# Performance work log

Hardware: AMD Instinct MI355X
Metric: run time of the kernel (lower is better)

The kernel has to match this reference:

```python
import jax, jax.numpy as jnp
import numpy as np

NIN = 4096
NOUT = 4096
LN_EPS = 1e-5  # torch.nn.LayerNorm default


def setup_inputs() -> dict:
    key = jax.random.key(0)
    ks = jax.random.split(key, 8)
    x = jax.random.normal(ks[0], (1, NIN), dtype=jnp.float32)
    hid = jax.random.normal(ks[1], (1, NOUT), dtype=jnp.float32)
    hebb = jnp.zeros((NOUT, NOUT), dtype=jnp.float32) + 1e-6  # initialZeroHebb
    # parameters
    w_in = 0.01 * jax.random.normal(ks[2], (NOUT, NIN), dtype=jnp.float32)  # inp_lin weight (no bias)
    w = 0.01 * jnp.eye(NOUT, NOUT, dtype=jnp.float32)                        # Plastic.w
    alpha = 0.01 * jax.random.normal(ks[3], (NOUT, NOUT), dtype=jnp.float32)
    b = 0.01 * jax.random.normal(ks[4], (NOUT,), dtype=jnp.float32)
    lamda = 0.01 * jnp.ones((1,), dtype=jnp.float32)
    pred_eta = 0.01 * jax.random.normal(ks[5], (NOUT, NOUT), dtype=jnp.float32)
    pred_eta_b = 0.01 * jax.random.normal(ks[6], (NOUT,), dtype=jnp.float32)
    ln_gamma = jnp.ones((NOUT,), dtype=jnp.float32)
    ln_beta = jnp.zeros((NOUT,), dtype=jnp.float32)
    return {"x": x, "hid": hid, "hebb": hebb, "w_in": w_in, "w": w,
            "alpha": alpha, "b": b, "lamda": lamda, "pred_eta": pred_eta,
            "pred_eta_b": pred_eta_b, "ln_gamma": ln_gamma, "ln_beta": ln_beta}


def reference(x, hid, hebb, w_in, w, alpha, b, lamda, pred_eta, pred_eta_b, ln_gamma, ln_beta):
    # Cell.forward (nonlin = ReLU for both wx and the post-LN output)
    wx = jax.nn.relu(x @ w_in.T)                       # [1, nout]
    wh = hid @ (w + alpha * hebb) + b                  # Plastic.forward, [1, nout]
    s = wx + wh
    mu = jnp.mean(s, axis=-1, keepdims=True)
    var = jnp.mean((s - mu) ** 2, axis=-1, keepdims=True)
    ln = ln_gamma * (s - mu) * jax.lax.rsqrt(var + LN_EPS) + ln_beta
    wy = jax.nn.relu(ln)                               # new hidden state, [1, nout]
    # Plastic.update_hebb(x=hid, y=wh, hebb)
    eta_hat = jax.nn.sigmoid(wh @ pred_eta + pred_eta_b)           # [1, nout]
    outer = hid[0, :, None] * wh[0, None, :]                        # [nout, nout]
    hebb_new = (1.0 - lamda) * hebb + eta_hat.T * outer             # row i scaled by eta_hat[0, i]
    return wy, hebb_new
```

## Files before the change

### kernel.cpp

```cpp
#include <hip/hip_runtime.h>
#include <hip/hip_bf16.h>
#include <math.h>

#define N 4096

__inline__ __device__ float waveReduceSum(float v) {
    #pragma unroll
    for (int o = 32; o > 0; o >>= 1) v += __shfl_down(v, o);
    return v;
}

__global__ __launch_bounds__(256) void k_wx(const float* __restrict__ x,
                                            const float* __restrict__ w_in,
                                            float* __restrict__ wx_out) {
    int j = blockIdx.x;
    const float4* row = reinterpret_cast<const float4*>(w_in + (size_t)j * N);
    const float4* xv  = reinterpret_cast<const float4*>(x);
    float sum = 0.f;
    #pragma unroll 4
    for (int k = threadIdx.x; k < N / 4; k += 256) {
        float4 a = row[k], c = xv[k];
        sum += a.x * c.x + a.y * c.y + a.z * c.z + a.w * c.w;
    }
    sum = waveReduceSum(sum);
    __shared__ float wsum[4];
    int wid = threadIdx.x >> 6, lane = threadIdx.x & 63;
    if (lane == 0) wsum[wid] = sum;
    __syncthreads();
    if (threadIdx.x == 0) {
        float t = wsum[0] + wsum[1] + wsum[2] + wsum[3];
        wx_out[j] = fmaxf(t, 0.f);
    }
}

__global__ __launch_bounds__(256) void k_wh_part(const float* __restrict__ hid,
                                                 const float* __restrict__ w,
                                                 const float* __restrict__ alpha,
                                                 const float* __restrict__ hebb,
                                                 float* __restrict__ part) {
    int j  = blockIdx.x * 256 + threadIdx.x;
    int i0 = blockIdx.y * 64;
    float sum = 0.f;
    #pragma unroll 4
    for (int i = i0; i < i0 + 64; ++i) {
        size_t off = (size_t)i * N + j;
        sum = fmaf(hid[i], fmaf(alpha[off], hebb[off], w[off]), sum);
    }
    part[(size_t)blockIdx.y * N + j] = sum;
}

__global__ __launch_bounds__(1024) void k_ln(const float* __restrict__ part,
                                             const float* __restrict__ b,
                                             const float* __restrict__ wx,
                                             const float* __restrict__ gamma,
                                             const float* __restrict__ beta,
                                             float* __restrict__ wh_out,
                                             float* __restrict__ wy_out) {
    __shared__ float red[16];
    __shared__ float bc[2];
    int tid = threadIdx.x;
    int wid = tid >> 6, lane = tid & 63;
    float sv[4];
    float lsum = 0.f;
    #pragma unroll
    for (int q = 0; q < 4; ++q) {
        int j = q * 1024 + tid;
        float acc = b[j];
        for (int c = 0; c < 64; ++c) acc += part[(size_t)c * N + j];
        wh_out[j] = acc;
        float s = acc + wx[j];
        sv[q] = s;
        lsum += s;
    }
    float wv = waveReduceSum(lsum);
    if (lane == 0) red[wid] = wv;
    __syncthreads();
    if (tid < 64) {
        float t = (tid < 16) ? red[tid] : 0.f;
        t = waveReduceSum(t);
        if (tid == 0) bc[0] = t * (1.f / N);
    }
    __syncthreads();
    float mean = bc[0];
    __syncthreads();
    float lsq = 0.f;
    #pragma unroll
    for (int q = 0; q < 4; ++q) { float d = sv[q] - mean; lsq += d * d; }
    wv = waveReduceSum(lsq);
    if (lane == 0) red[wid] = wv;
    __syncthreads();
    if (tid < 64) {
        float t = (tid < 16) ? red[tid] : 0.f;
        t = waveReduceSum(t);
        if (tid == 0) bc[1] = t * (1.f / N);
    }
    __syncthreads();
    float rstd = rsqrtf(bc[1] + 1e-5f);
    #pragma unroll
    for (int q = 0; q < 4; ++q) {
        int j = q * 1024 + tid;
        float ln = fmaf(gamma[j] * (sv[q] - mean), rstd, beta[j]);
        wy_out[j] = fmaxf(ln, 0.f);
    }
}

__global__ __launch_bounds__(256) void k_eta_part(const float* __restrict__ wh,
                                                  const float* __restrict__ pe,
                                                  float* __restrict__ part) {
    int j  = blockIdx.x * 256 + threadIdx.x;
    int i0 = blockIdx.y * 64;
    float sum = 0.f;
    #pragma unroll 4
    for (int i = i0; i < i0 + 64; ++i) {
        sum = fmaf(wh[i], pe[(size_t)i * N + j], sum);
    }
    part[(size_t)blockIdx.y * N + j] = sum;
}

__global__ __launch_bounds__(256) void k_eta_fin(const float* __restrict__ part,
                                                 const float* __restrict__ pb,
                                                 float* __restrict__ eta) {
    int j = blockIdx.x * 256 + threadIdx.x;
    float s = pb[j];
    for (int c = 0; c < 64; ++c) s += part[(size_t)c * N + j];
    eta[j] = 1.f / (1.f + expf(-s));
}

__global__ __launch_bounds__(256) void k_hebb(const float* __restrict__ hebb,
                                              const float* __restrict__ eta,
                                              const float* __restrict__ hid,
                                              const float* __restrict__ wh,
                                              const float* __restrict__ lamda,
                                              float* __restrict__ out) {
    int i  = blockIdx.y;
    int j0 = blockIdx.x * 1024 + threadIdx.x * 4;
    float decay = 1.f - lamda[0];
    float coef  = eta[i] * hid[i];
    const float4 h  = *reinterpret_cast<const float4*>(hebb + (size_t)i * N + j0);
    const float4 w4 = *reinterpret_cast<const float4*>(wh + j0);
    float4 r;
    r.x = fmaf(decay, h.x, coef * w4.x);
    r.y = fmaf(decay, h.y, coef * w4.y);
    r.z = fmaf(decay, h.z, coef * w4.z);
    r.w = fmaf(decay, h.w, coef * w4.w);
    *reinterpret_cast<float4*>(out + (size_t)i * N + j0) = r;
}

extern "C" void kernel_launch(void* const* d_in, const int* in_sizes, int n_in,
                              void* d_out, int out_size, void* d_ws, size_t ws_size,
                              hipStream_t stream) {
    const float* x         = (const float*)d_in[0];
    const float* hid       = (const float*)d_in[1];
    const float* hebb      = (const float*)d_in[2];
    const float* w_in      = (const float*)d_in[3];
    const float* w         = (const float*)d_in[4];
    const float* alpha     = (const float*)d_in[5];
    const float* b         = (const float*)d_in[6];
    const float* lamda     = (const float*)d_in[7];
    const float* pred_eta  = (const float*)d_in[8];
    const float* pred_eta_b= (const float*)d_in[9];
    const float* ln_gamma  = (const float*)d_in[10];
    const float* ln_beta   = (const float*)d_in[11];

    float* wy       = (float*)d_out;
    float* hebb_out = (float*)d_out + N;

    float* ws   = (float*)d_ws;
    float* part = ws;
    float* wx   = ws + 64 * N;
    float* wh   = ws + 64 * N + N;
    float* eta  = ws + 64 * N + 2 * N;

    k_wx      <<<N, 256, 0, stream>>>(x, w_in, wx);
    k_wh_part <<<dim3(16, 64), 256, 0, stream>>>(hid, w, alpha, hebb, part);
    k_ln      <<<1, 1024, 0, stream>>>(part, b, wx, ln_gamma, ln_beta, wh, wy);
    k_eta_part<<<dim3(16, 64), 256, 0, stream>>>(wh, pred_eta, part);
    k_eta_fin <<<16, 256, 0, stream>>>(part, pred_eta_b, eta);
    k_hebb    <<<dim3(4, N), 256, 0, stream>>>(hebb, eta, hid, wh, lamda, hebb_out);
}
```

Baseline: 106.6 us.

## Vectorize split-K matvecs with float4, double chunk count, parallelize wh reduction

The column-wise split-K matvec kernels for wh and eta now load float4 per thread with 4 columns each and use 128 row chunks of 32 instead of 64 chunks of 64. The partial-sum reduction for wh moves out of the single-block layernorm kernel into its own 16-block kernel, so the serial 64-deep reduction in one block no longer sits on the critical path. The aim is wider memory transactions and more parallelism in the reductions, at the cost of one extra launch and twice the partial-buffer traffic.

```diff
diff --git a/kernel.cpp b/kernel.cpp
--- a/kernel.cpp
+++ b/kernel.cpp
@@ -3,6 +3,8 @@
 #include <math.h>
 
 #define N 4096
+#define CHUNK 32
+#define NCHUNK (N / CHUNK)
 
 __inline__ __device__ float waveReduceSum(float v) {
     #pragma unroll
@@ -17,7 +19,7 @@
     const float4* row = reinterpret_cast<const float4*>(w_in + (size_t)j * N);
     const float4* xv  = reinterpret_cast<const float4*>(x);
     float sum = 0.f;
-    #pragma unroll 4
+    #pragma unroll
     for (int k = threadIdx.x; k < N / 4; k += 256) {
         float4 a = row[k], c = xv[k];
         sum += a.x * c.x + a.y * c.y + a.z * c.z + a.w * c.w;
@@ -38,23 +40,41 @@
                                                  const float* __restrict__ alpha,
                                                  const float* __restrict__ hebb,
                                                  float* __restrict__ part) {
-    int j  = blockIdx.x * 256 + threadIdx.x;
-    int i0 = blockIdx.y * 64;
-    float sum = 0.f;
+    int j0 = blockIdx.x * 1024 + threadIdx.x * 4;
+    int i0 = blockIdx.y * CHUNK;
+    const float4* w4 = reinterpret_cast<const float4*>(w);
+    const float4* a4 = reinterpret_cast<const float4*>(alpha);
+    const float4* h4 = reinterpret_cast<const float4*>(hebb);
+    float4 acc = make_float4(0.f, 0.f, 0.f, 0.f);
     #pragma unroll 4
-    for (int i = i0; i < i0 + 64; ++i) {
-        size_t off = (size_t)i * N + j;
-        sum = fmaf(hid[i], fmaf(alpha[off], hebb[off], w[off]), sum);
-    }
-    part[(size_t)blockIdx.y * N + j] = sum;
-}
-
-__global__ __launch_bounds__(1024) void k_ln(const float* __restrict__ part,
-                                             const float* __restrict__ b,
+    for (int i = i0; i < i0 + CHUNK; ++i) {
+        size_t idx = ((size_t)i * N + j0) >> 2;
+        float4 wv = w4[idx];
+        float4 av = a4[idx];
+        float4 hv = h4[idx];
+        float  h  = hid[i];
+        acc.x = fmaf(h, fmaf(av.x, hv.x, wv.x), acc.x);
+        acc.y = fmaf(h, fmaf(av.y, hv.y, wv.y), acc.y);
+        acc.z = fmaf(h, fmaf(av.z, hv.z, wv.z), acc.z);
+        acc.w = fmaf(h, fmaf(av.w, hv.w, wv.w), acc.w);
+    }
+    *reinterpret_cast<float4*>(part + (size_t)blockIdx.y * N + j0) = acc;
+}
+
+__global__ __launch_bounds__(256) void k_wh_fin(const float* __restrict__ part,
+                                                const float* __restrict__ b,
+                                                float* __restrict__ wh) {
+    int j = blockIdx.x * 256 + threadIdx.x;
+    float s = b[j];
+    #pragma unroll 8
+    for (int c = 0; c < NCHUNK; ++c) s += part[(size_t)c * N + j];
+    wh[j] = s;
+}
+
+__global__ __launch_bounds__(1024) void k_ln(const float* __restrict__ wh,
                                              const float* __restrict__ wx,
                                              const float* __restrict__ gamma,
                                              const float* __restrict__ beta,
-                                             float* __restrict__ wh_out,
                                              float* __restrict__ wy_out) {
     __shared__ float red[16];
     __shared__ float bc[2];
@@ -65,10 +85,7 @@
     #pragma unroll
     for (int q = 0; q < 4; ++q) {
         int j = q * 1024 + tid;
-        float acc = b[j];
-        for (int c = 0; c < 64; ++c) acc += part[(size_t)c * N + j];
-        wh_out[j] = acc;
-        float s = acc + wx[j];
+        float s = wh[j] + wx[j];
         sv[q] = s;
         lsum += s;
     }
@@ -107,14 +124,21 @@
 __global__ __launch_bounds__(256) void k_eta_part(const float* __restrict__ wh,
                                                   const float* __restrict__ pe,
                                                   float* __restrict__ part) {
-    int j  = blockIdx.x * 256 + threadIdx.x;
-    int i0 = blockIdx.y * 64;
-    float sum = 0.f;
+    int j0 = blockIdx.x * 1024 + threadIdx.x * 4;
+    int i0 = blockIdx.y * CHUNK;
+    const float4* p4 = reinterpret_cast<const float4*>(pe);
+    float4 acc = make_float4(0.f, 0.f, 0.f, 0.f);
     #pragma unroll 4
-    for (int i = i0; i < i0 + 64; ++i) {
-        sum = fmaf(wh[i], pe[(size_t)i * N + j], sum);
-    }
-    part[(size_t)blockIdx.y * N + j] = sum;
+    for (int i = i0; i < i0 + CHUNK; ++i) {
+        size_t idx = ((size_t)i * N + j0) >> 2;
+        float4 pv = p4[idx];
+        float  h  = wh[i];
+        acc.x = fmaf(h, pv.x, acc.x);
+        acc.y = fmaf(h, pv.y, acc.y);
+        acc.z = fmaf(h, pv.z, acc.z);
+        acc.w = fmaf(h, pv.w, acc.w);
+    }
+    *reinterpret_cast<float4*>(part + (size_t)blockIdx.y * N + j0) = acc;
 }
 
 __global__ __launch_bounds__(256) void k_eta_fin(const float* __restrict__ part,
@@ -122,7 +146,8 @@
                                                  float* __restrict__ eta) {
     int j = blockIdx.x * 256 + threadIdx.x;
     float s = pb[j];
-    for (int c = 0; c < 64; ++c) s += part[(size_t)c * N + j];
+    #pragma unroll 8
+    for (int c = 0; c < NCHUNK; ++c) s += part[(size_t)c * N + j];
     eta[j] = 1.f / (1.f + expf(-s));
 }
 
@@ -167,14 +192,15 @@
 
     float* ws   = (float*)d_ws;
     float* part = ws;
-    float* wx   = ws + 64 * N;
-    float* wh   = ws + 64 * N + N;
-    float* eta  = ws + 64 * N + 2 * N;
+    float* wx   = ws + NCHUNK * N;
+    float* wh   = ws + NCHUNK * N + N;
+    float* eta  = ws + NCHUNK * N + 2 * N;
 
     k_wx      <<<N, 256, 0, stream>>>(x, w_in, wx);
-    k_wh_part <<<dim3(16, 64), 256, 0, stream>>>(hid, w, alpha, hebb, part);
-    k_ln      <<<1, 1024, 0, stream>>>(part, b, wx, ln_gamma, ln_beta, wh, wy);
-    k_eta_part<<<dim3(16, 64), 256, 0, stream>>>(wh, pred_eta, part);
+    k_wh_part <<<dim3(4, NCHUNK), 256, 0, stream>>>(hid, w, alpha, hebb, part);
+    k_wh_fin  <<<16, 256, 0, stream>>>(part, b, wh);
+    k_ln      <<<1, 1024, 0, stream>>>(wh, wx, ln_gamma, ln_beta, wy);
+    k_eta_part<<<dim3(4, NCHUNK), 256, 0, stream>>>(wh, pred_eta, part);
     k_eta_fin <<<16, 256, 0, stream>>>(part, pred_eta_b, eta);
     k_hebb    <<<dim3(4, N), 256, 0, stream>>>(hebb, eta, hid, wh, lamda, hebb_out);
 }
```

After: 103.8 us. 1.03x faster.

## Fuse wx and wh GEMVs into one launch with finer row chunks and two-level reduction

Applied to the files above, without the earlier changes.

Merges the w_in GEMV and the plastic-weight GEMV into a single kernel whose blocks are split between the two jobs. The column-wise GEMVs now use float4 loads and smaller row chunks (8 or 32, chosen by workspace size), giving many more blocks. The resulting partial sums go through a separate two-level reduction kernel. The hebb update now has one block per row with 16 elements per thread. This removes a launch and improves occupancy and load width, at the cost of a larger partial-sum buffer and extra reduction launches.

```diff
diff --git a/kernel.cpp b/kernel.cpp
--- a/kernel.cpp
+++ b/kernel.cpp
@@ -3,6 +3,7 @@
 #include <math.h>
 
 #define N 4096
+#define NGRP 16
 
 __inline__ __device__ float waveReduceSum(float v) {
     #pragma unroll
@@ -10,46 +11,99 @@
     return v;
 }
 
-__global__ __launch_bounds__(256) void k_wx(const float* __restrict__ x,
-                                            const float* __restrict__ w_in,
-                                            float* __restrict__ wx_out) {
-    int j = blockIdx.x;
-    const float4* row = reinterpret_cast<const float4*>(w_in + (size_t)j * N);
-    const float4* xv  = reinterpret_cast<const float4*>(x);
-    float sum = 0.f;
-    #pragma unroll 4
-    for (int k = threadIdx.x; k < N / 4; k += 256) {
-        float4 a = row[k], c = xv[k];
-        sum += a.x * c.x + a.y * c.y + a.z * c.z + a.w * c.w;
-    }
-    sum = waveReduceSum(sum);
-    __shared__ float wsum[4];
-    int wid = threadIdx.x >> 6, lane = threadIdx.x & 63;
-    if (lane == 0) wsum[wid] = sum;
-    __syncthreads();
-    if (threadIdx.x == 0) {
-        float t = wsum[0] + wsum[1] + wsum[2] + wsum[3];
-        wx_out[j] = fmaxf(t, 0.f);
-    }
-}
-
-__global__ __launch_bounds__(256) void k_wh_part(const float* __restrict__ hid,
-                                                 const float* __restrict__ w,
-                                                 const float* __restrict__ alpha,
-                                                 const float* __restrict__ hebb,
-                                                 float* __restrict__ part) {
-    int j  = blockIdx.x * 256 + threadIdx.x;
-    int i0 = blockIdx.y * 64;
-    float sum = 0.f;
-    #pragma unroll 4
-    for (int i = i0; i < i0 + 64; ++i) {
-        size_t off = (size_t)i * N + j;
-        sum = fmaf(hid[i], fmaf(alpha[off], hebb[off], w[off]), sum);
-    }
-    part[(size_t)blockIdx.y * N + j] = sum;
-}
-
-__global__ __launch_bounds__(1024) void k_ln(const float* __restrict__ part,
+template<int CHUNK>
+__global__ __launch_bounds__(256) void k_combo1(const float* __restrict__ x,
+                                                const float* __restrict__ w_in,
+                                                const float* __restrict__ hid,
+                                                const float* __restrict__ w,
+                                                const float* __restrict__ alpha,
+                                                const float* __restrict__ hebb,
+                                                float* __restrict__ part,
+                                                float* __restrict__ wx_out,
+                                                int nWh) {
+    if ((int)blockIdx.x < nWh) {
+        int bid = blockIdx.x;
+        int xt  = bid & 3;
+        int cy  = bid >> 2;
+        int j0  = xt * 1024 + threadIdx.x * 4;
+        int i0  = cy * CHUNK;
+        float hv[CHUNK];
+        #pragma unroll
+        for (int r = 0; r < CHUNK; ++r) hv[r] = hid[i0 + r];
+        float4 acc = make_float4(0.f, 0.f, 0.f, 0.f);
+        #pragma unroll
+        for (int r = 0; r < CHUNK; ++r) {
+            size_t off = (size_t)(i0 + r) * N + j0;
+            float4 wv = *reinterpret_cast<const float4*>(w + off);
+            float4 av = *reinterpret_cast<const float4*>(alpha + off);
+            float4 bv = *reinterpret_cast<const float4*>(hebb + off);
+            acc.x = fmaf(hv[r], fmaf(av.x, bv.x, wv.x), acc.x);
+            acc.y = fmaf(hv[r], fmaf(av.y, bv.y, wv.y), acc.y);
+            acc.z = fmaf(hv[r], fmaf(av.z, bv.z, wv.z), acc.z);
+            acc.w = fmaf(hv[r], fmaf(av.w, bv.w, wv.w), acc.w);
+        }
+        *reinterpret_cast<float4*>(part + (size_t)cy * N + j0) = acc;
+    } else {
+        int j = blockIdx.x - nWh;
+        const float4* row = reinterpret_cast<const float4*>(w_in + (size_t)j * N);
+        const float4* xv  = reinterpret_cast<const float4*>(x);
+        float sum = 0.f;
+        #pragma unroll
+        for (int k = threadIdx.x; k < N / 4; k += 256) {
+            float4 a = row[k], c = xv[k];
+            sum += a.x * c.x + a.y * c.y + a.z * c.z + a.w * c.w;
+        }
+        sum = waveReduceSum(sum);
+        __shared__ float wsum[4];
+        int wid = threadIdx.x >> 6, lane = threadIdx.x & 63;
+        if (lane == 0) wsum[wid] = sum;
+        __syncthreads();
+        if (threadIdx.x == 0)
+            wx_out[j] = fmaxf(wsum[0] + wsum[1] + wsum[2] + wsum[3], 0.f);
+    }
+}
+
+template<int CHUNK>
+__global__ __launch_bounds__(256) void k_eta_part(const float* __restrict__ wh,
+                                                  const float* __restrict__ pe,
+                                                  float* __restrict__ part) {
+    int bid = blockIdx.x;
+    int xt  = bid & 3;
+    int cy  = bid >> 2;
+    int j0  = xt * 1024 + threadIdx.x * 4;
+    int i0  = cy * CHUNK;
+    float hv[CHUNK];
+    #pragma unroll
+    for (int r = 0; r < CHUNK; ++r) hv[r] = wh[i0 + r];
+    float4 acc = make_float4(0.f, 0.f, 0.f, 0.f);
+    #pragma unroll
+    for (int r = 0; r < CHUNK; ++r) {
+        size_t off = (size_t)(i0 + r) * N + j0;
+        float4 pv = *reinterpret_cast<const float4*>(pe + off);
+        acc.x = fmaf(hv[r], pv.x, acc.x);
+        acc.y = fmaf(hv[r], pv.y, acc.y);
+        acc.z = fmaf(hv[r], pv.z, acc.z);
+        acc.w = fmaf(hv[r], pv.w, acc.w);
+    }
+    *reinterpret_cast<float4*>(part + (size_t)cy * N + j0) = acc;
+}
+
+__global__ __launch_bounds__(256) void k_red(const float* __restrict__ part,
+                                             float* __restrict__ part2,
+                                             int cpg) {
+    int g  = blockIdx.y;
+    int j0 = (blockIdx.x * 256 + threadIdx.x) * 4;
+    const float4* p4 = reinterpret_cast<const float4*>(part);
+    float4 s = make_float4(0.f, 0.f, 0.f, 0.f);
+    #pragma unroll 8
+    for (int c = 0; c < cpg; ++c) {
+        float4 v = p4[((size_t)(g * cpg + c) * N + j0) >> 2];
+        s.x += v.x; s.y += v.y; s.z += v.z; s.w += v.w;
+    }
+    *reinterpret_cast<float4*>(part2 + (size_t)g * N + j0) = s;
+}
+
+__global__ __launch_bounds__(1024) void k_ln(const float* __restrict__ part2,
                                              const float* __restrict__ b,
                                              const float* __restrict__ wx,
                                              const float* __restrict__ gamma,
@@ -66,7 +120,8 @@
     for (int q = 0; q < 4; ++q) {
         int j = q * 1024 + tid;
         float acc = b[j];
-        for (int c = 0; c < 64; ++c) acc += part[(size_t)c * N + j];
+        #pragma unroll
+        for (int g = 0; g < NGRP; ++g) acc += part2[(size_t)g * N + j];
         wh_out[j] = acc;
         float s = acc + wx[j];
         sv[q] = s;
@@ -104,26 +159,22 @@
     }
 }
 
-__global__ __launch_bounds__(256) void k_eta_part(const float* __restrict__ wh,
-                                                  const float* __restrict__ pe,
-                                                  float* __restrict__ part) {
-    int j  = blockIdx.x * 256 + threadIdx.x;
-    int i0 = blockIdx.y * 64;
-    float sum = 0.f;
-    #pragma unroll 4
-    for (int i = i0; i < i0 + 64; ++i) {
-        sum = fmaf(wh[i], pe[(size_t)i * N + j], sum);
-    }
-    part[(size_t)blockIdx.y * N + j] = sum;
-}
-
-__global__ __launch_bounds__(256) void k_eta_fin(const float* __restrict__ part,
+__global__ __launch_bounds__(256) void k_eta_fin(const float* __restrict__ part2,
                                                  const float* __restrict__ pb,
                                                  float* __restrict__ eta) {
-    int j = blockIdx.x * 256 + threadIdx.x;
-    float s = pb[j];
-    for (int c = 0; c < 64; ++c) s += part[(size_t)c * N + j];
-    eta[j] = 1.f / (1.f + expf(-s));
+    int j0 = (blockIdx.x * 256 + threadIdx.x) * 4;
+    float4 s = *reinterpret_cast<const float4*>(pb + j0);
+    #pragma unroll
+    for (int g = 0; g < NGRP; ++g) {
+        float4 v = *reinterpret_cast<const float4*>(part2 + (size_t)g * N + j0);
+        s.x += v.x; s.y += v.y; s.z += v.z; s.w += v.w;
+    }
+    float4 r;
+    r.x = 1.f / (1.f + expf(-s.x));
+    r.y = 1.f / (1.f + expf(-s.y));
+    r.z = 1.f / (1.f + expf(-s.z));
+    r.w = 1.f / (1.f + expf(-s.w));
+    *reinterpret_cast<float4*>(eta + j0) = r;
 }
 
 __global__ __launch_bounds__(256) void k_hebb(const float* __restrict__ hebb,
@@ -132,18 +183,23 @@
                                               const float* __restrict__ wh,
                                               const float* __restrict__ lamda,
                                               float* __restrict__ out) {
-    int i  = blockIdx.y;
-    int j0 = blockIdx.x * 1024 + threadIdx.x * 4;
+    int i  = blockIdx.x;
     float decay = 1.f - lamda[0];
     float coef  = eta[i] * hid[i];
-    const float4 h  = *reinterpret_cast<const float4*>(hebb + (size_t)i * N + j0);
-    const float4 w4 = *reinterpret_cast<const float4*>(wh + j0);
-    float4 r;
-    r.x = fmaf(decay, h.x, coef * w4.x);
-    r.y = fmaf(decay, h.y, coef * w4.y);
-    r.z = fmaf(decay, h.z, coef * w4.z);
-    r.w = fmaf(decay, h.w, coef * w4.w);
-    *reinterpret_cast<float4*>(out + (size_t)i * N + j0) = r;
+    size_t base = (size_t)i * N;
+    int j0 = threadIdx.x * 16;
+    #pragma unroll
+    for (int q = 0; q < 4; ++q) {
+        int j = j0 + q * 4;
+        float4 h  = *reinterpret_cast<const float4*>(hebb + base + j);
+        float4 w4 = *reinterpret_cast<const float4*>(wh + j);
+        float4 r;
+        r.x = fmaf(decay, h.x, coef * w4.x);
+        r.y = fmaf(decay, h.y, coef * w4.y);
+        r.z = fmaf(decay, h.z, coef * w4.z);
+        r.w = fmaf(decay, h.w, coef * w4.w);
+        *reinterpret_cast<float4*>(out + base + j) = r;
+    }
 }
 
 extern "C" void kernel_launch(void* const* d_in, const int* in_sizes, int n_in,
@@ -165,16 +221,34 @@
     float* wy       = (float*)d_out;
     float* hebb_out = (float*)d_out + N;
 
-    float* ws   = (float*)d_ws;
-    float* part = ws;
-    float* wx   = ws + 64 * N;
-    float* wh   = ws + 64 * N + N;
-    float* eta  = ws + 64 * N + 2 * N;
-
-    k_wx      <<<N, 256, 0, stream>>>(x, w_in, wx);
-    k_wh_part <<<dim3(16, 64), 256, 0, stream>>>(hid, w, alpha, hebb, part);
-    k_ln      <<<1, 1024, 0, stream>>>(part, b, wx, ln_gamma, ln_beta, wh, wy);
-    k_eta_part<<<dim3(16, 64), 256, 0, stream>>>(wh, pred_eta, part);
-    k_eta_fin <<<16, 256, 0, stream>>>(part, pred_eta_b, eta);
-    k_hebb    <<<dim3(4, N), 256, 0, stream>>>(hebb, eta, hid, wh, lamda, hebb_out);
-}
+    const size_t needF8 = ((size_t)(N / 8) * N) + (size_t)NGRP * N + 3 * N;
+    bool big = (ws_size / 4) >= needF8;
+
+    float* ws = (float*)d_ws;
+    int nchunk = big ? (N / 8) : (N / 32);
+    float* part  = ws;
+    float* part2 = ws + (size_t)nchunk * N;
+    float* wx    = part2 + (size_t)NGRP * N;
+    float* wh    = wx + N;
+    float* eta   = wh + N;
+    int cpg = nchunk / NGRP;
+
+    if (big) {
+        int nWh = 4 * (N / 8);
+        k_combo1<8><<<nWh + N, 256, 0, stream>>>(x, w_in, hid, w, alpha, hebb, part, wx, nWh);
+        k_red    <<<dim3(4, NGRP), 256, 0, stream>>>(part, part2, cpg);
+        k_ln     <<<1, 1024, 0, stream>>>(part2, b, wx, ln_gamma, ln_beta, wh, wy);
+        k_eta_part<8><<<nWh, 256, 0, stream>>>(wh, pred_eta, part);
+        k_red    <<<dim3(4, NGRP), 256, 0, stream>>>(part, part2, cpg);
+        k_eta_fin<<<4, 256, 0, stream>>>(part2, pred_eta_b, eta);
+    } else {
+        int nWh = 4 * (N / 32);
+        k_combo1<32><<<nWh + N, 256, 0, stream>>>(x, w_in, hid, w, alpha, hebb, part, wx, nWh);
+        k_red    <<<dim3(4, NGRP), 256, 0, stream>>>(part, part2, cpg);
+        k_ln     <<<1, 1024, 0, stream>>>(part2, b, wx, ln_gamma, ln_beta, wh, wy);
+        k_eta_part<32><<<nWh, 256, 0, stream>>>(wh, pred_eta, part);
+        k_red    <<<dim3(4, NGRP), 256, 0, stream>>>(part, part2, cpg);
+        k_eta_fin<<<4, 256, 0, stream>>>(part2, pred_eta_b, eta);
+    }
+    k_hebb<<<N, 256, 0, stream>>>(hebb, eta, hid, wh, lamda, hebb_out);
+}
```

Result: slower. 109.7 us (+2.9%).

## Restructure matrix sweeps into grid-strided float4 streaming with hierarchical reduction

Applied to the files above, without the earlier changes.

Replaces the per-row and per-column-block kernels with grid-strided sweeps where G blocks each stream whole 1024-float row chunks using float4 loads. Partial sums are reduced in two stages (an extra reduction kernel plus the final kernel) instead of one 64-way serial loop. The hebb update is made persistent and uses nontemporal stores. The goal is to cut launch count and per-block overhead and raise memory streaming efficiency, at the cost of larger workspace, extra kernel launches, and a sync-heavy wx kernel.

```diff
diff --git a/kernel.cpp b/kernel.cpp
--- a/kernel.cpp
+++ b/kernel.cpp
@@ -3,6 +3,10 @@
 #include <math.h>
 
 #define N 4096
+#define NGRP 16
+#define NF4 (N * (N / 4))
+
+typedef float f32x4 __attribute__((ext_vector_type(4)));
 
 __inline__ __device__ float waveReduceSum(float v) {
     #pragma unroll
@@ -10,48 +14,101 @@
     return v;
 }
 
-__global__ __launch_bounds__(256) void k_wx(const float* __restrict__ x,
-                                            const float* __restrict__ w_in,
-                                            float* __restrict__ wx_out) {
-    int j = blockIdx.x;
-    const float4* row = reinterpret_cast<const float4*>(w_in + (size_t)j * N);
-    const float4* xv  = reinterpret_cast<const float4*>(x);
-    float sum = 0.f;
-    #pragma unroll 4
-    for (int k = threadIdx.x; k < N / 4; k += 256) {
-        float4 a = row[k], c = xv[k];
-        sum += a.x * c.x + a.y * c.y + a.z * c.z + a.w * c.w;
-    }
-    sum = waveReduceSum(sum);
-    __shared__ float wsum[4];
-    int wid = threadIdx.x >> 6, lane = threadIdx.x & 63;
-    if (lane == 0) wsum[wid] = sum;
-    __syncthreads();
-    if (threadIdx.x == 0) {
-        float t = wsum[0] + wsum[1] + wsum[2] + wsum[3];
-        wx_out[j] = fmaxf(t, 0.f);
-    }
-}
-
-__global__ __launch_bounds__(256) void k_wh_part(const float* __restrict__ hid,
-                                                 const float* __restrict__ w,
-                                                 const float* __restrict__ alpha,
-                                                 const float* __restrict__ hebb,
-                                                 float* __restrict__ part) {
-    int j  = blockIdx.x * 256 + threadIdx.x;
-    int i0 = blockIdx.y * 64;
-    float sum = 0.f;
-    #pragma unroll 4
-    for (int i = i0; i < i0 + 64; ++i) {
-        size_t off = (size_t)i * N + j;
-        sum = fmaf(hid[i], fmaf(alpha[off], hebb[off], w[off]), sum);
-    }
-    part[(size_t)blockIdx.y * N + j] = sum;
-}
-
-__global__ __launch_bounds__(1024) void k_ln(const float* __restrict__ part,
+#define LD4(p, o) (*reinterpret_cast<const float4*>((p) + (o)))
+
+__global__ __launch_bounds__(256) void k_sweep_wh(const float* __restrict__ hid,
+                                                  const float* __restrict__ w,
+                                                  const float* __restrict__ alpha,
+                                                  const float* __restrict__ hebb,
+                                                  float* __restrict__ part,
+                                                  int G, int iters) {
+    int b = blockIdx.x, t = threadIdx.x;
+    int p = b >> 2;
+    int j0 = (((b & 3) << 8) | t) * 4;
+    int P = G >> 2;
+    float4 acc = make_float4(0.f, 0.f, 0.f, 0.f);
+    size_t step = (size_t)G * 1024;
+    size_t off = (size_t)(((b << 8) | t)) * 4;
+    #pragma unroll 8
+    for (int k = 0; k < iters; ++k, off += step) {
+        float h = hid[k * P + p];
+        float4 wv = LD4(w, off);
+        float4 av = LD4(alpha, off);
+        float4 hv = LD4(hebb, off);
+        acc.x = fmaf(h, fmaf(av.x, hv.x, wv.x), acc.x);
+        acc.y = fmaf(h, fmaf(av.y, hv.y, wv.y), acc.y);
+        acc.z = fmaf(h, fmaf(av.z, hv.z, wv.z), acc.z);
+        acc.w = fmaf(h, fmaf(av.w, hv.w, wv.w), acc.w);
+    }
+    *reinterpret_cast<float4*>(part + (size_t)p * N + j0) = acc;
+}
+
+__global__ __launch_bounds__(256) void k_sweep_eta(const float* __restrict__ wh,
+                                                   const float* __restrict__ pe,
+                                                   float* __restrict__ part,
+                                                   int G, int iters) {
+    int b = blockIdx.x, t = threadIdx.x;
+    int p = b >> 2;
+    int j0 = (((b & 3) << 8) | t) * 4;
+    int P = G >> 2;
+    float4 acc = make_float4(0.f, 0.f, 0.f, 0.f);
+    size_t step = (size_t)G * 1024;
+    size_t off = (size_t)(((b << 8) | t)) * 4;
+    #pragma unroll 8
+    for (int k = 0; k < iters; ++k, off += step) {
+        float h = wh[k * P + p];
+        float4 pv = LD4(pe, off);
+        acc.x = fmaf(h, pv.x, acc.x);
+        acc.y = fmaf(h, pv.y, acc.y);
+        acc.z = fmaf(h, pv.z, acc.z);
+        acc.w = fmaf(h, pv.w, acc.w);
+    }
+    *reinterpret_cast<float4*>(part + (size_t)p * N + j0) = acc;
+}
+
+__global__ __launch_bounds__(256) void k_sweep_wx(const float* __restrict__ x,
+                                                  const float* __restrict__ w_in,
+                                                  float* __restrict__ part_wx,
+                                                  int G, int iters) {
+    __shared__ float red[4];
+    int b = blockIdx.x, t = threadIdx.x;
+    int p = b >> 2;
+    int P = G >> 2;
+    int j0 = (((b & 3) << 8) | t) * 4;
+    float4 xv = LD4(x, j0);
+    size_t step = (size_t)G * 1024;
+    size_t off = (size_t)(((b << 8) | t)) * 4;
+    int wid = t >> 6, lane = t & 63;
+    for (int k = 0; k < iters; ++k, off += step) {
+        float4 wv = LD4(w_in, off);
+        float d = wv.x * xv.x + wv.y * xv.y + wv.z * xv.z + wv.w * xv.w;
+        d = waveReduceSum(d);
+        if (lane == 0) red[wid] = d;
+        __syncthreads();
+        if (t == 0)
+            part_wx[(size_t)(b & 3) * N + (k * P + p)] = red[0] + red[1] + red[2] + red[3];
+        __syncthreads();
+    }
+}
+
+__global__ __launch_bounds__(256) void k_red(const float* __restrict__ part,
+                                             float* __restrict__ part2,
+                                             int cpg) {
+    int g  = blockIdx.y;
+    int j0 = (blockIdx.x * 256 + threadIdx.x) * 4;
+    const float4* p4 = reinterpret_cast<const float4*>(part);
+    float4 s = make_float4(0.f, 0.f, 0.f, 0.f);
+    #pragma unroll 8
+    for (int c = 0; c < cpg; ++c) {
+        float4 v = p4[((size_t)(g * cpg + c) * N + j0) >> 2];
+        s.x += v.x; s.y += v.y; s.z += v.z; s.w += v.w;
+    }
+    *reinterpret_cast<float4*>(part2 + (size_t)g * N + j0) = s;
+}
+
+__global__ __launch_bounds__(1024) void k_ln(const float* __restrict__ part2,
+                                             const float* __restrict__ part_wx,
                                              const float* __restrict__ b,
-                                             const float* __restrict__ wx,
                                              const float* __restrict__ gamma,
                                              const float* __restrict__ beta,
                                              float* __restrict__ wh_out,
@@ -66,9 +123,11 @@
     for (int q = 0; q < 4; ++q) {
         int j = q * 1024 + tid;
         float acc = b[j];
-        for (int c = 0; c < 64; ++c) acc += part[(size_t)c * N + j];
+        #pragma unroll
+        for (int g = 0; g < NGRP; ++g) acc += part2[(size_t)g * N + j];
         wh_out[j] = acc;
-        float s = acc + wx[j];
+        float wx = part_wx[j] + part_wx[N + j] + part_wx[2 * N + j] + part_wx[3 * N + j];
+        float s = acc + fmaxf(wx, 0.f);
         sv[q] = s;
         lsum += s;
     }
@@ -104,26 +163,22 @@
     }
 }
 
-__global__ __launch_bounds__(256) void k_eta_part(const float* __restrict__ wh,
-                                                  const float* __restrict__ pe,
-                                                  float* __restrict__ part) {
-    int j  = blockIdx.x * 256 + threadIdx.x;
-    int i0 = blockIdx.y * 64;
-    float sum = 0.f;
-    #pragma unroll 4
-    for (int i = i0; i < i0 + 64; ++i) {
-        sum = fmaf(wh[i], pe[(size_t)i * N + j], sum);
-    }
-    part[(size_t)blockIdx.y * N + j] = sum;
-}
-
-__global__ __launch_bounds__(256) void k_eta_fin(const float* __restrict__ part,
+__global__ __launch_bounds__(256) void k_eta_fin(const float* __restrict__ part2,
                                                  const float* __restrict__ pb,
                                                  float* __restrict__ eta) {
-    int j = blockIdx.x * 256 + threadIdx.x;
-    float s = pb[j];
-    for (int c = 0; c < 64; ++c) s += part[(size_t)c * N + j];
-    eta[j] = 1.f / (1.f + expf(-s));
+    int j0 = (blockIdx.x * 256 + threadIdx.x) * 4;
+    float4 s = *reinterpret_cast<const float4*>(pb + j0);
+    #pragma unroll
+    for (int g = 0; g < NGRP; ++g) {
+        float4 v = *reinterpret_cast<const float4*>(part2 + (size_t)g * N + j0);
+        s.x += v.x; s.y += v.y; s.z += v.z; s.w += v.w;
+    }
+    float4 r;
+    r.x = 1.f / (1.f + expf(-s.x));
+    r.y = 1.f / (1.f + expf(-s.y));
+    r.z = 1.f / (1.f + expf(-s.z));
+    r.w = 1.f / (1.f + expf(-s.w));
+    *reinterpret_cast<float4*>(eta + j0) = r;
 }
 
 __global__ __launch_bounds__(256) void k_hebb(const float* __restrict__ hebb,
@@ -131,19 +186,28 @@
                                               const float* __restrict__ hid,
                                               const float* __restrict__ wh,
                                               const float* __restrict__ lamda,
-                                              float* __restrict__ out) {
-    int i  = blockIdx.y;
-    int j0 = blockIdx.x * 1024 + threadIdx.x * 4;
+                                              float* __restrict__ out,
+                                              int G, int iters) {
+    int b = blockIdx.x, t = threadIdx.x;
+    int p = b >> 2;
+    int P = G >> 2;
+    int j0 = (((b & 3) << 8) | t) * 4;
     float decay = 1.f - lamda[0];
-    float coef  = eta[i] * hid[i];
-    const float4 h  = *reinterpret_cast<const float4*>(hebb + (size_t)i * N + j0);
-    const float4 w4 = *reinterpret_cast<const float4*>(wh + j0);
-    float4 r;
-    r.x = fmaf(decay, h.x, coef * w4.x);
-    r.y = fmaf(decay, h.y, coef * w4.y);
-    r.z = fmaf(decay, h.z, coef * w4.z);
-    r.w = fmaf(decay, h.w, coef * w4.w);
-    *reinterpret_cast<float4*>(out + (size_t)i * N + j0) = r;
+    float4 w4 = LD4(wh, j0);
+    size_t step = (size_t)G * 1024;
+    size_t off = (size_t)(((b << 8) | t)) * 4;
+    #pragma unroll 4
+    for (int k = 0; k < iters; ++k, off += step) {
+        int i = k * P + p;
+        float coef = eta[i] * hid[i];
+        float4 h = LD4(hebb, off);
+        f32x4 r;
+        r.x = fmaf(decay, h.x, coef * w4.x);
+        r.y = fmaf(decay, h.y, coef * w4.y);
+        r.z = fmaf(decay, h.z, coef * w4.z);
+        r.w = fmaf(decay, h.w, coef * w4.w);
+        __builtin_nontemporal_store(r, reinterpret_cast<f32x4*>(out + off));
+    }
 }
 
 extern "C" void kernel_launch(void* const* d_in, const int* in_sizes, int n_in,
@@ -165,16 +229,25 @@
     float* wy       = (float*)d_out;
     float* hebb_out = (float*)d_out + N;
 
-    float* ws   = (float*)d_ws;
-    float* part = ws;
-    float* wx   = ws + 64 * N;
-    float* wh   = ws + 64 * N + N;
-    float* eta  = ws + 64 * N + 2 * N;
-
-    k_wx      <<<N, 256, 0, stream>>>(x, w_in, wx);
-    k_wh_part <<<dim3(16, 64), 256, 0, stream>>>(hid, w, alpha, hebb, part);
-    k_ln      <<<1, 1024, 0, stream>>>(part, b, wx, ln_gamma, ln_beta, wh, wy);
-    k_eta_part<<<dim3(16, 64), 256, 0, stream>>>(wh, pred_eta, part);
-    k_eta_fin <<<16, 256, 0, stream>>>(part, pred_eta_b, eta);
-    k_hebb    <<<dim3(4, N), 256, 0, stream>>>(hebb, eta, hid, wh, lamda, hebb_out);
-}
+    int G = 2048;
+    if ((ws_size / 4) < ((size_t)(G / 4) * N + (NGRP + 6) * N)) G = 512;
+    int P = G / 4;
+    int iters = NF4 / (G * 256);
+    int cpg = P / NGRP;
+
+    float* ws      = (float*)d_ws;
+    float* part    = ws;
+    float* part2   = part + (size_t)P * N;
+    float* part_wx = part2 + (size_t)NGRP * N;
+    float* wh      = part_wx + 4 * N;
+    float* eta     = wh + N;
+
+    k_sweep_wx <<<G, 256, 0, stream>>>(x, w_in, part_wx, G, iters);
+    k_sweep_wh <<<G, 256, 0, stream>>>(hid, w, alpha, hebb, part, G, iters);
+    k_red      <<<dim3(4, NGRP), 256, 0, stream>>>(part, part2, cpg);
+    k_ln       <<<1, 1024, 0, stream>>>(part2, part_wx, b, ln_gamma, ln_beta, wh, wy);
+    k_sweep_eta<<<G, 256, 0, stream>>>(wh, pred_eta, part, G, iters);
+    k_red      <<<dim3(4, NGRP), 256, 0, stream>>>(part, part2, cpg);
+    k_eta_fin  <<<4, 256, 0, stream>>>(part2, pred_eta_b, eta);
+    k_hebb     <<<G, 256, 0, stream>>>(hebb, eta, hid, wh, lamda, hebb_out, G, iters);
+}
```

Result: no change. 107.7 us (+1.0%).
